# Kernel optimization log

Hardware: AMD Instinct MI355X
Metric: run time of the kernel (lower is better)

Reference implementation:

```python
import jax, jax.numpy as jnp
import numpy as np

NEG = -1e9  # large negative instead of -inf for numerical safety; masked rows are zeroed afterwards
LN_EPS = 1e-5


def layer_norm(x, g, b):
    mu = jnp.mean(x, axis=-1, keepdims=True)
    var = jnp.mean(jnp.square(x - mu), axis=-1, keepdims=True)
    return (x - mu) * jax.lax.rsqrt(var + LN_EPS) * g + b


def causal_conv1d(x_bct, w_oik):
    # x: [B, C, T], w: [O, I, K]; left-pad by K-1 (causal ConvNorm)
    k = w_oik.shape[-1]
    return jax.lax.conv_general_dilated(
        x_bct, w_oik, window_strides=(1,), padding=[(k - 1, 0)],
        dimension_numbers=('NCH', 'OIH', 'NCH'))


def setup_inputs() -> dict:
    key = jax.random.key(0)
    ks = jax.random.split(key, 8)
    B, T, D, H, F, K = 2, 2048, 1024, 16, 4096, 3
    MAXLEN = 4096
    x = jax.random.normal(ks[0], (B, T, D), dtype=jnp.float32)
    lengths = jnp.array([2048, 1536])
    x_mask = jnp.arange(T)[None, :] >= lengths[:, None]  # True = padded
    std = 0.02
    pos_table = jax.random.normal(ks[1], (MAXLEN, D), dtype=jnp.float32) * std
    w_qkv = jax.random.normal(ks[2], (3 * D, D), dtype=jnp.float32) * std
    w_o = jax.random.normal(ks[3], (D, D), dtype=jnp.float32) * std
    conv1_w = jax.random.normal(ks[4], (F, D, K), dtype=jnp.float32) * std
    conv2_w = jax.random.normal(ks[5], (D, F, K), dtype=jnp.float32) * std
    return {
        'x': x, 'x_mask': x_mask, 'pos_table': pos_table,
        'w_qkv': w_qkv, 'w_o': w_o,
        'ln1_g': jnp.ones((D,)), 'ln1_b': jnp.zeros((D,)),
        'ln2_g': jnp.ones((D,)), 'ln2_b': jnp.zeros((D,)),
        'conv1_w': conv1_w, 'conv2_w': conv2_w,
    }


def reference(x, x_mask, pos_table, w_qkv, w_o, ln1_g, ln1_b, ln2_g, ln2_b, conv1_w, conv2_w):
    B, T, D = x.shape
    H = 16
    dh = D // H
    scale = dh ** -0.5

    # ---- self-attention block (pre-norm) ----
    q_in = layer_norm(x, ln1_g, ln1_b)
    q_in = q_in + pos_table[:T][None]  # learnable positional embeddings
    qkv = jnp.einsum('btd,ed->bte', q_in, w_qkv).reshape(B, T, 3, H, dh)
    q, k, v = qkv[:, :, 0], qkv[:, :, 1], qkv[:, :, 2]
    scores = jnp.einsum('bthd,bshd->bhts', q, k) * scale  # [B,H,T,T]
    pad_mask = x_mask[:, None, :, None]                    # mask padded query rows
    causal = jnp.tril(jnp.ones((T, T), dtype=bool))[None, None]
    scores = jnp.where(pad_mask | ~causal, NEG, scores)
    prob = jax.nn.softmax(scores, axis=-1)
    prob = jnp.where(pad_mask, 0.0, prob)
    y = jnp.einsum('bhts,bshd->bthd', prob, v).reshape(B, T, D)
    y = jnp.einsum('btd,ed->bte', y, w_o)
    x = x + y  # dropout p=0

    # ---- positionwise causal conv FFN (pre-norm) ----
    h = layer_norm(x, ln2_g, ln2_b)
    h = jnp.transpose(h, (0, 2, 1))           # [B, D, T]
    h = causal_conv1d(h, conv1_w)             # [B, F, T]
    h = jax.nn.gelu(h, approximate=True)
    h = causal_conv1d(h, conv2_w)             # [B, D, T]
    h = jnp.transpose(h, (0, 2, 1))
    x = x + h
    return x
```

## Files before the change

kernel.cpp:

```cpp
#include <hip/hip_runtime.h>
#include <stdint.h>
#include <math.h>

#define T_SEQ 2048
#define D_MODEL 1024
#define NHEAD 16
#define DH 64
#define F_FF 4096
#define TP (T_SEQ + 2)

typedef unsigned short u16;
typedef float f32x4 __attribute__((ext_vector_type(4)));
typedef __bf16 bf16x8 __attribute__((ext_vector_type(8)));

__device__ __forceinline__ u16 f2bf(float f){
  unsigned u = __float_as_uint(f);
  u = u + 0x7fffu + ((u >> 16) & 1u);
  return (u16)(u >> 16);
}
__device__ __forceinline__ float b2f(u16 h){ return __uint_as_float(((unsigned)h) << 16); }

__device__ __forceinline__ float gelu_f(float x){
  const float c = 0.7978845608028654f;
  float u = c * (x + 0.044715f * x * x * x);
  float e = __expf(-2.0f * u);
  return x * __builtin_amdgcn_rcpf(1.0f + e);
}

#define AS1 __attribute__((address_space(1)))
#define AS3 __attribute__((address_space(3)))
__device__ __forceinline__ void async_cp16(void* lds, const void* g){
  __builtin_amdgcn_global_load_lds((AS1 void*)(void*)g, (AS3 void*)lds, 16, 0, 0);
}

__device__ __forceinline__ float fload(const void* p, size_t i, unsigned isbf){
  return isbf ? b2f(((const u16*)p)[i]) : ((const float*)p)[i];
}

__global__ void detect_dtype(const u16* __restrict__ x, unsigned* __restrict__ flags){
  unsigned e = ((unsigned)x[threadIdx.x] >> 7) & 0xFF;
  bool good = (e == 0 || (e >= 90 && e <= 150));
  unsigned long long b = __ballot(good);
  if (threadIdx.x == 0) flags[0] = (b == ~0ULL) ? 1u : 0u;
}

__global__ __launch_bounds__(256) void canon_mask(const unsigned char* __restrict__ raw,
                                                  unsigned char* __restrict__ canon){
  int i = blockIdx.x * 256 + threadIdx.x;
  if (i >= 2 * T_SEQ) return;
  unsigned char v;
  if (raw[3584]) {
    v = raw[i] != 0;
  } else if (raw[7168]) {
    v = ((const u16*)raw)[i] != 0;
  } else if (raw[14336]) {
    v = ((const int*)raw)[i] != 0;
  } else {
    v = ((const long long*)raw)[i] != 0;
  }
  canon[i] = v;
}

__global__ __launch_bounds__(256)
void cast_any2bf(const void* __restrict__ in, u16* __restrict__ out, int n,
                 const unsigned* __restrict__ flags){
  int i = (blockIdx.x * 256 + threadIdx.x) * 4;
  if (i >= n) return;
  if (flags[0]){
    *(ushort4*)(out + i) = *(const ushort4*)((const u16*)in + i);
  } else {
    float4 v = *(const float4*)((const float*)in + i);
    ushort4 o = { f2bf(v.x), f2bf(v.y), f2bf(v.z), f2bf(v.w) };
    *(ushort4*)(out + i) = o;
  }
}

__global__ __launch_bounds__(256)
void cast_out(const float* __restrict__ in, const float* __restrict__ res,
              void* __restrict__ out, int n, const unsigned* __restrict__ flags){
  int i = (blockIdx.x * 256 + threadIdx.x) * 4;
  if (i >= n) return;
  float4 v = *(const float4*)(in + i);
  float4 r = *(const float4*)(res + i);
  v.x += r.x; v.y += r.y; v.z += r.z; v.w += r.w;
  if (flags[0]){
    ushort4 o = { f2bf(v.x), f2bf(v.y), f2bf(v.z), f2bf(v.w) };
    *(ushort4*)((u16*)out + i) = o;
  } else {
    *(float4*)((float*)out + i) = v;
  }
}

template<int INX1>
__global__ __launch_bounds__(256)
void ln_kernel(const void* __restrict__ inv, const void* __restrict__ g,
               const void* __restrict__ be, const void* __restrict__ pos,
               u16* __restrict__ out, int addpos, int padout,
               const unsigned* __restrict__ flags)
{
  const unsigned isbf = flags[0];
  const int r = blockIdx.x;
  const int bb = r >> 11, tt = r & (T_SEQ - 1);
  const size_t ib = (size_t)r * D_MODEL + threadIdx.x * 4;
  float v0, v1, v2, v3;
  if (INX1){
    float4 v = *(const float4*)((const float*)inv + ib);
    v0 = v.x; v1 = v.y; v2 = v.z; v3 = v.w;
  } else if (isbf){
    ushort4 u = *(const ushort4*)((const u16*)inv + ib);
    v0 = b2f(u.x); v1 = b2f(u.y); v2 = b2f(u.z); v3 = b2f(u.w);
  } else {
    float4 v = *(const float4*)((const float*)inv + ib);
    v0 = v.x; v1 = v.y; v2 = v.z; v3 = v.w;
  }
  float s  = v0 + v1 + v2 + v3;
  float s2 = v0*v0 + v1*v1 + v2*v2 + v3*v3;
  #pragma unroll
  for (int o = 1; o < 64; o <<= 1){ s += __shfl_xor(s, o); s2 += __shfl_xor(s2, o); }
  __shared__ float w1[4], w2[4];
  int w = threadIdx.x >> 6;
  if ((threadIdx.x & 63) == 0){ w1[w] = s; w2[w] = s2; }
  __syncthreads();
  float S  = w1[0] + w1[1] + w1[2] + w1[3];
  float S2 = w2[0] + w2[1] + w2[2] + w2[3];
  float mu  = S * (1.f / 1024.f);
  float var = S2 * (1.f / 1024.f) - mu * mu;
  float rs  = rsqrtf(var + 1e-5f);
  int d0 = threadIdx.x * 4;
  float o0 = (v0 - mu) * rs * fload(g, d0 + 0, isbf) + fload(be, d0 + 0, isbf);
  float o1 = (v1 - mu) * rs * fload(g, d0 + 1, isbf) + fload(be, d0 + 1, isbf);
  float o2 = (v2 - mu) * rs * fload(g, d0 + 2, isbf) + fload(be, d0 + 2, isbf);
  float o3 = (v3 - mu) * rs * fload(g, d0 + 3, isbf) + fload(be, d0 + 3, isbf);
  if (addpos){
    size_t pb = (size_t)tt * D_MODEL + d0;
    o0 += fload(pos, pb + 0, isbf);
    o1 += fload(pos, pb + 1, isbf);
    o2 += fload(pos, pb + 2, isbf);
    o3 += fload(pos, pb + 3, isbf);
  }
  size_t orow = padout ? ((size_t)bb * TP + tt + 2) * (size_t)D_MODEL
                       : (size_t)r * D_MODEL;
  ushort4 ov = { f2bf(o0), f2bf(o1), f2bf(o2), f2bf(o3) };
  *(ushort4*)(out + orow + d0) = ov;
}

__global__ __launch_bounds__(256)
void conv_w_split(const void* __restrict__ in, u16* __restrict__ out, int lg2C,
                  const unsigned* __restrict__ flags){
  int i = blockIdx.x * 256 + threadIdx.x;
  if (i >= 4096 * 1024) return;
  const unsigned isbf = flags[0];
  const int C = 1 << lg2C;
  int c = i & (C - 1);
  size_t sb = (size_t)i * 3;
  size_t ob = (size_t)(i >> lg2C) * 3 * C + c;
  out[ob]         = f2bf(fload(in, sb + 0, isbf));
  out[ob + C]     = f2bf(fload(in, sb + 1, isbf));
  out[ob + 2 * C] = f2bf(fload(in, sb + 2, isbf));
}

__global__ __launch_bounds__(256)
void zero_pads(u16* __restrict__ h2pad, u16* __restrict__ g1pad){
  int tid = blockIdx.x * 256 + threadIdx.x;
  if (tid < 2 * 2 * D_MODEL){
    int b = tid >> 11; int off = tid & (2 * D_MODEL - 1);
    h2pad[(size_t)b * TP * D_MODEL + off] = 0;
  }
  if (tid < 2 * 2 * F_FF){
    int b = tid >> 13; int off = tid & (2 * F_FF - 1);
    g1pad[(size_t)b * TP * F_FF + off] = 0;
  }
}

__device__ __forceinline__ int swz(int tid){
  return (tid & 3) ^ ((tid >> 2) & 3) ^ ((tid >> 4) & 3);
}

template<int MODE>
__global__ __launch_bounds__(256)
void gemm_bt(const u16* __restrict__ A, const u16* __restrict__ B,
             const void* __restrict__ res, void* __restrict__ outp,
             int N, int Kin, int lg2Kin, int nseg, long Abstride,
             const unsigned* __restrict__ flags)
{
  __shared__ u16 smA[128 * 32];
  __shared__ u16 smB[128 * 32];
  const int tid = threadIdx.x;
  const int m0 = blockIdx.y * 128;
  const int n0 = blockIdx.x * 128;
  const int Ktot = Kin * nseg;

  const int ch = swz(tid);
  long abase[2]; const u16* bbase[2];
  #pragma unroll
  for (int i = 0; i < 2; ++i){
    int r = m0 + i * 64 + (tid >> 2);
    int bb = r >> 11, tt = r & (T_SEQ - 1);
    abase[i] = (long)bb * Abstride + (long)tt * Kin + ch * 8;
    bbase[i] = B + (long)(n0 + i * 64 + (tid >> 2)) * Ktot + ch * 8;
  }

  f32x4 acc[4][4];
  #pragma unroll
  for (int i = 0; i < 4; ++i)
    #pragma unroll
    for (int j = 0; j < 4; ++j){ f32x4 z = {0.f,0.f,0.f,0.f}; acc[i][j] = z; }

  const int wm = (tid >> 6) & 1, wn = (tid >> 7) & 1;
  const int lane = tid & 63, lq = lane >> 4, lr = lane & 15;
  const int xq = lq ^ (lr & 3) ^ (lr >> 2);
  const int aoff = (wm * 64 + lr) * 32 + xq * 8;
  const int boff = (wn * 64 + lr) * 32 + xq * 8;

  for (int k0 = 0; k0 < Ktot; k0 += 32){
    int seg = k0 >> lg2Kin;
    int j0  = k0 & (Kin - 1);
    long aso = (long)seg * Kin + j0;
    long bso = k0;
    #pragma unroll
    for (int i = 0; i < 2; ++i){
      async_cp16(&smA[i * 2048 + tid * 8], A + abase[i] + aso);
      async_cp16(&smB[i * 2048 + tid * 8], bbase[i] + bso);
    }
    __syncthreads();
    bf16x8 af[4], bfv[4];
    #pragma unroll
    for (int mi = 0; mi < 4; ++mi) af[mi]  = *(const bf16x8*)&smA[aoff + mi * 512];
    #pragma unroll
    for (int ni = 0; ni < 4; ++ni) bfv[ni] = *(const bf16x8*)&smB[boff + ni * 512];
    #pragma unroll
    for (int mi = 0; mi < 4; ++mi)
      #pragma unroll
      for (int ni = 0; ni < 4; ++ni)
        acc[mi][ni] = __builtin_amdgcn_mfma_f32_16x16x32_bf16(af[mi], bfv[ni], acc[mi][ni], 0, 0, 0);
    __syncthreads();
  }

  const unsigned isbf = (MODE == 1 || MODE == 3) ? flags[0] : 0;
  #pragma unroll
  for (int mi = 0; mi < 4; ++mi){
    #pragma unroll
    for (int ni = 0; ni < 4; ++ni){
      int row0 = m0 + wm * 64 + mi * 16 + lq * 4;
      int col  = n0 + wn * 64 + ni * 16 + lr;
      if (MODE == 0){
        ushort4 pv = { f2bf(acc[mi][ni][0]), f2bf(acc[mi][ni][1]),
                       f2bf(acc[mi][ni][2]), f2bf(acc[mi][ni][3]) };
        if (col < 2 * D_MODEL){
          #pragma unroll
          for (int rr = 0; rr < 4; ++rr)
            ((u16*)outp)[(size_t)(row0 + rr) * N + col] = ((const u16*)&pv)[rr];
        } else {
          int hh = (col - 2 * D_MODEL) >> 6, dd = (col - 2 * D_MODEL) & 63;
          int bb = row0 >> 11, tt = row0 & (T_SEQ - 1);
          *(ushort4*)((u16*)const_cast<void*>(res) +
                      ((size_t)(bb * NHEAD + hh) * 64 + dd) * T_SEQ + tt) = pv;
        }
      } else {
        #pragma unroll
        for (int rr = 0; rr < 4; ++rr){
          int row = row0 + rr;
          float v = acc[mi][ni][rr];
          size_t idx = (size_t)row * N + col;
          if (MODE == 1){
            ((float*)outp)[idx] = v + fload(res, idx, isbf);
          } else if (MODE == 3){
            float ov = v + ((const float*)res)[idx];
            if (isbf) ((u16*)outp)[idx] = f2bf(ov);
            else      ((float*)outp)[idx] = ov;
          }
        }
      }
    }
  }
}

__device__ __forceinline__ void ktile8(
    f32x4 (&acc)[8][4], u16 (*L)[16384], int buf, int abase, int bbase,
    const u16* __restrict__ A, const long (&asrc)[2], const u16* const (&bsrc)[2],
    const int (&adst)[2], const int (&bdst)[2], int kt, bool stage_ok)
{
  const u16* Lp = L[buf];
  u16* Ld = L[(kt + 3) & 3];
  bf16x8 bfr[4], a0[4], a1[4];
  #pragma unroll
  for (int nf = 0; nf < 4; ++nf) bfr[nf] = *(const bf16x8*)&Lp[bbase + nf * 512];
  #pragma unroll
  for (int j = 0; j < 4; ++j) a0[j] = *(const bf16x8*)&Lp[abase + j * 512];
  if (stage_ok){
    #pragma unroll
    for (int s = 0; s < 2; ++s)
      async_cp16(&Ld[adst[s]], A + asrc[s] + (long)(kt + 3) * 32);
  }
  #pragma unroll
  for (int j = 0; j < 4; ++j) a1[j] = *(const bf16x8*)&Lp[abase + (4 + j) * 512];
  if (stage_ok){
    #pragma unroll
    for (int s = 0; s < 2; ++s)
      async_cp16(&Ld[bdst[s]], bsrc[s] + (long)(kt + 3) * 32);
  }
  __builtin_amdgcn_s_setprio(1);
  #pragma unroll
  for (int j = 0; j < 4; ++j)
    #pragma unroll
    for (int nf = 0; nf < 4; ++nf)
      acc[j][nf] = __builtin_amdgcn_mfma_f32_16x16x32_bf16(a0[j], bfr[nf], acc[j][nf], 0, 0, 0);
  #pragma unroll
  for (int j = 0; j < 4; ++j)
    #pragma unroll
    for (int nf = 0; nf < 4; ++nf)
      acc[4 + j][nf] = __builtin_amdgcn_mfma_f32_16x16x32_bf16(a1[j], bfr[nf], acc[4 + j][nf], 0, 0, 0);
  __builtin_amdgcn_s_setprio(0);
}

template<int MODE>
__global__ __launch_bounds__(512, 2)
void gemm8(const u16* __restrict__ A, const u16* __restrict__ Bm,
           void* __restrict__ outp, int N, int Kin, int Ktot, int nkt, long Abstride)
{
  __shared__ u16 L[4][16384];
  const int tid = threadIdx.x;

  const int bid = blockIdx.x;
  const int xcd = bid & 7, idx = bid >> 3;
  int bx, by, kz;
  if (MODE == 2){ bx = 2 * xcd + (idx & 1); by = idx >> 1; kz = 0; }
  else          { kz = xcd >> 1; bx = idx & 3; by = ((xcd & 1) << 3) + (idx >> 2); }
  const int m0 = by * 256, n0 = bx * 256;
  const int kt0 = kz * nkt;
  const int ktEnd = kt0 + nkt;

  const int rl = tid >> 2;
  const int ch = swz(tid);
  long asrc[2]; const u16* bsrc[2]; int adst[2], bdst[2];
  #pragma unroll
  for (int s = 0; s < 2; ++s){
    int r = m0 + s * 128 + rl;
    int bb = r >> 11, tt = r & (T_SEQ - 1);
    asrc[s] = (long)bb * Abstride + (long)tt * Kin + ch * 8;
    bsrc[s] = Bm + (long)(n0 + s * 128 + rl) * Ktot + ch * 8;
    adst[s] = (s * 512 + tid) * 8;
    bdst[s] = 8192 + adst[s];
  }

  const int w = tid >> 6, lane = tid & 63;
  const int wm = w >> 2, wn = w & 3;
  const int quad = lane >> 4, lr = lane & 15;
  const int xq = quad ^ (lr & 3) ^ (lr >> 2);
  const int abase = ((wm * 128 + lr) * 4 + xq) * 8;
  const int bbase = 8192 + ((wn * 64 + lr) * 4 + xq) * 8;

  f32x4 acc[8][4];
  #pragma unroll
  for (int i = 0; i < 8; ++i)
    #pragma unroll
    for (int j = 0; j < 4; ++j){ f32x4 z = {0.f,0.f,0.f,0.f}; acc[i][j] = z; }

  #pragma unroll
  for (int j = 0; j < 3; ++j){
    #pragma unroll
    for (int s = 0; s < 2; ++s) async_cp16(&L[(kt0 + j) & 3][adst[s]], A + asrc[s] + (long)(kt0 + j) * 32);
    #pragma unroll
    for (int s = 0; s < 2; ++s) async_cp16(&L[(kt0 + j) & 3][bdst[s]], bsrc[s] + (long)(kt0 + j) * 32);
  }

  int kt = kt0;
  for (; kt < ktEnd - 2; ++kt){
    asm volatile("s_waitcnt vmcnt(8)" ::: "memory");
    __builtin_amdgcn_s_barrier();
    __builtin_amdgcn_sched_barrier(0);
    ktile8(acc, L, kt & 3, abase, bbase, A, asrc, bsrc, adst, bdst, kt, kt + 3 < ktEnd);
  }
  asm volatile("s_waitcnt vmcnt(4)" ::: "memory");
  __builtin_amdgcn_s_barrier();
  __builtin_amdgcn_sched_barrier(0);
  ktile8(acc, L, (ktEnd - 2) & 3, abase, bbase, A, asrc, bsrc, adst, bdst, ktEnd - 2, false);
  asm volatile("s_waitcnt vmcnt(0)" ::: "memory");
  __builtin_amdgcn_s_barrier();
  __builtin_amdgcn_sched_barrier(0);
  ktile8(acc, L, (ktEnd - 1) & 3, abase, bbase, A, asrc, bsrc, adst, bdst, ktEnd - 1, false);

  #pragma unroll
  for (int mf = 0; mf < 8; ++mf){
    #pragma unroll
    for (int nf = 0; nf < 4; ++nf){
      int col = n0 + wn * 64 + nf * 16 + lr;
      #pragma unroll
      for (int rr = 0; rr < 4; ++rr){
        int row = m0 + wm * 128 + mf * 16 + quad * 4 + rr;
        if (MODE == 2){
          int bb = row >> 11, tt = row & (T_SEQ - 1);
          ((u16*)outp)[((size_t)(bb * TP + tt + 2)) * N + col] = f2bf(gelu_f(acc[mf][nf][rr]));
        } else {
          atomicAdd((float*)outp + (size_t)row * N + col, acc[mf][nf][rr]);
        }
      }
    }
  }
}

__global__ __launch_bounds__(256)
void attn_mfma(const u16* __restrict__ qkv, const u16* __restrict__ vT,
               const unsigned char* __restrict__ mask, u16* __restrict__ y)
{
  const int qb = blockIdx.x, h = blockIdx.y, b = blockIdx.z;
  const int q0 = qb * 64;
  const int tid = threadIdx.x;

  if (mask[b * T_SEQ + q0]){
    int r = tid >> 2, c4 = (tid & 3) * 16;
    u16* yp = y + (size_t)(b * T_SEQ + q0 + r) * D_MODEL + h * DH + c4;
    ushort4 z = {0, 0, 0, 0};
    #pragma unroll
    for (int c = 0; c < 4; ++c) *(ushort4*)(yp + c * 4) = z;
    return;
  }

  const int w = tid >> 6, lane = tid & 63;
  const int quad = lane >> 4, lr = lane & 15;

  __shared__ u16 Ks[64 * 72];
  __shared__ u16 Vs[64 * 72];
  __shared__ u16 Ps[64 * 72];

  bf16x8 aq0, aq1;
  {
    const u16* qp = qkv + (size_t)(b * T_SEQ + q0 + w * 16 + lr) * 3072 + h * DH + quad * 8;
    aq0 = *(const bf16x8*)qp;
    aq1 = *(const bf16x8*)(qp + 32);
  }

  f32x4 acc_o[4];
  #pragma unroll
  for (int i = 0; i < 4; ++i){ f32x4 z = {0.f,0.f,0.f,0.f}; acc_o[i] = z; }
  float mrow[4] = {-1e30f, -1e30f, -1e30f, -1e30f};
  float lrow[4] = {0.f, 0.f, 0.f, 0.f};

  const int sr = tid >> 3, sg = tid & 7;

  for (int it = 0; it <= qb; ++it){
    const int s0 = it * 64;
    #pragma unroll
    for (int rr = 0; rr < 64; rr += 32){
      int row = sr + rr;
      *(uint4*)&Ks[row * 72 + sg * 8] =
        *(const uint4*)(qkv + (size_t)(b * T_SEQ + s0 + row) * 3072 + D_MODEL + h * DH + sg * 8);
      *(uint4*)&Vs[row * 72 + sg * 8] =
        *(const uint4*)(vT + ((size_t)(b * NHEAD + h) * 64 + row) * T_SEQ + s0 + sg * 8);
    }
    __syncthreads();

    f32x4 accs[4];
    #pragma unroll
    for (int nt = 0; nt < 4; ++nt){
      f32x4 z = {0.f, 0.f, 0.f, 0.f};
      bf16x8 bk0 = *(const bf16x8*)&Ks[(nt * 16 + lr) * 72 + quad * 8];
      bf16x8 bk1 = *(const bf16x8*)&Ks[(nt * 16 + lr) * 72 + quad * 8 + 32];
      z = __builtin_amdgcn_mfma_f32_16x16x32_bf16(aq0, bk0, z, 0, 0, 0);
      z = __builtin_amdgcn_mfma_f32_16x16x32_bf16(aq1, bk1, z, 0, 0, 0);
      accs[nt] = z;
    }

    const bool diag = (it == qb);
    float sv[4][4], mx[4];
    #pragma unroll
    for (int rr = 0; rr < 4; ++rr) mx[rr] = -1e30f;
    #pragma unroll
    for (int nt = 0; nt < 4; ++nt){
      #pragma unroll
      for (int rr = 0; rr < 4; ++rr){
        float s = accs[nt][rr] * 0.125f;
        if (diag && (nt * 16 + lr) > (w * 16 + quad * 4 + rr)) s = -1e30f;
        sv[nt][rr] = s;
        mx[rr] = fmaxf(mx[rr], s);
      }
    }
    #pragma unroll
    for (int o = 1; o < 16; o <<= 1){
      #pragma unroll
      for (int rr = 0; rr < 4; ++rr) mx[rr] = fmaxf(mx[rr], __shfl_xor(mx[rr], o));
    }
    float alpha[4], psum[4];
    #pragma unroll
    for (int rr = 0; rr < 4; ++rr){
      float mnew = fmaxf(mrow[rr], mx[rr]);
      alpha[rr] = __expf(mrow[rr] - mnew);
      mrow[rr] = mnew;
      psum[rr] = 0.f;
    }
    #pragma unroll
    for (int nt = 0; nt < 4; ++nt){
      #pragma unroll
      for (int rr = 0; rr < 4; ++rr){
        float p = __expf(sv[nt][rr] - mrow[rr]);
        psum[rr] += p;
        Ps[(w * 16 + quad * 4 + rr) * 72 + nt * 16 + lr] = f2bf(p);
      }
    }
    #pragma unroll
    for (int o = 1; o < 16; o <<= 1){
      #pragma unroll
      for (int rr = 0; rr < 4; ++rr) psum[rr] += __shfl_xor(psum[rr], o);
    }
    #pragma unroll
    for (int rr = 0; rr < 4; ++rr) lrow[rr] = lrow[rr] * alpha[rr] + psum[rr];
    #pragma unroll
    for (int nt = 0; nt < 4; ++nt)
      #pragma unroll
      for (int rr = 0; rr < 4; ++rr) acc_o[nt][rr] *= alpha[rr];

    bf16x8 ap0 = *(const bf16x8*)&Ps[(w * 16 + lr) * 72 + quad * 8];
    bf16x8 ap1 = *(const bf16x8*)&Ps[(w * 16 + lr) * 72 + quad * 8 + 32];
    #pragma unroll
    for (int nt = 0; nt < 4; ++nt){
      bf16x8 bv0 = *(const bf16x8*)&Vs[(nt * 16 + lr) * 72 + quad * 8];
      bf16x8 bv1 = *(const bf16x8*)&Vs[(nt * 16 + lr) * 72 + quad * 8 + 32];
      acc_o[nt] = __builtin_amdgcn_mfma_f32_16x16x32_bf16(ap0, bv0, acc_o[nt], 0, 0, 0);
      acc_o[nt] = __builtin_amdgcn_mfma_f32_16x16x32_bf16(ap1, bv1, acc_o[nt], 0, 0, 0);
    }
    __syncthreads();
  }

  #pragma unroll
  for (int rr = 0; rr < 4; ++rr){
    int qg = q0 + w * 16 + quad * 4 + rr;
    float inv = 1.0f / lrow[rr];
    bool rm = mask[b * T_SEQ + qg] != 0;
    #pragma unroll
    for (int nt = 0; nt < 4; ++nt){
      float v = rm ? 0.f : acc_o[nt][rr] * inv;
      y[(size_t)(b * T_SEQ + qg) * D_MODEL + h * DH + nt * 16 + lr] = f2bf(v);
    }
  }
}

extern "C" void kernel_launch(void* const* d_in, const int* in_sizes, int n_in,
                              void* d_out, int out_size, void* d_ws, size_t ws_size,
                              hipStream_t stream)
{
  const void* x       = d_in[0];
  const unsigned char* xmask_raw = (const unsigned char*)d_in[1];
  const void* pos     = d_in[2];
  const void* w_qkv   = d_in[3];
  const void* w_o     = d_in[4];
  const void* ln1_g   = d_in[5];
  const void* ln1_b   = d_in[6];
  const void* ln2_g   = d_in[7];
  const void* ln2_b   = d_in[8];
  const void* conv1_w = d_in[9];
  const void* conv2_w = d_in[10];

  char* ws = (char*)d_ws;
  size_t o = 0;
  auto alloc = [&](size_t bytes){ size_t cur = o; o += (bytes + 255) & ~(size_t)255; return cur; };
  unsigned* flags = (unsigned*)(ws + alloc(256));
  unsigned char* maskc = (unsigned char*)(ws + alloc(2 * T_SEQ));
  float* x1   = (float*)(ws + alloc((size_t)2 * T_SEQ * D_MODEL * 4));
  char* h2slab = ws + alloc((size_t)2 * TP * D_MODEL * 2);
  u16* g1pad  = (u16*)(ws + alloc((size_t)2 * TP * F_FF * 2));
  u16* slabA  = (u16*)(ws + alloc((size_t)4096 * 3072 * 2));
  u16* qy     = (u16*)(ws + alloc((size_t)4096 * 1024 * 2));
  char* vslab = ws + alloc((size_t)4096 * 1024 * 4);
  u16* vt     = (u16*)vslab;
  float* xc   = (float*)vslab;

  u16* wqkv_c = (u16*)h2slab;
  u16* wo_c   = (u16*)h2slab + (size_t)3072 * 1024;
  u16* h2pad  = (u16*)h2slab;
  u16* qin    = qy;
  u16* qkvb   = slabA;
  u16* yb     = qy;
  u16* W1cat  = slabA;
  u16* W2cat  = slabA;

  detect_dtype<<<1, 64, 0, stream>>>((const u16*)x, flags);
  canon_mask<<<16, 256, 0, stream>>>(xmask_raw, maskc);
  cast_any2bf<<<3072 * 1024 / 4 / 256, 256, 0, stream>>>(w_qkv, wqkv_c, 3072 * 1024, flags);
  cast_any2bf<<<1024 * 1024 / 4 / 256, 256, 0, stream>>>(w_o, wo_c, 1024 * 1024, flags);
  ln_kernel<0><<<4096, 256, 0, stream>>>(x, ln1_g, ln1_b, pos, qin, 1, 0, flags);
  gemm_bt<0><<<dim3(24, 32), 256, 0, stream>>>(qin, wqkv_c, vt, qkvb,
                                               3072, 1024, 10, 1, (long)T_SEQ * 1024, flags);
  attn_mfma<<<dim3(32, 16, 2), 256, 0, stream>>>(qkvb, vt, maskc, yb);
  gemm_bt<1><<<dim3(8, 32), 256, 0, stream>>>(yb, wo_c, x, x1,
                                              1024, 1024, 10, 1, (long)T_SEQ * 1024, flags);
  hipMemsetAsync(xc, 0, (size_t)4096 * 1024 * 4, stream);
  conv_w_split<<<4096 * 1024 / 256, 256, 0, stream>>>(conv1_w, W1cat, 10, flags);
  zero_pads<<<64, 256, 0, stream>>>(h2pad, g1pad);
  ln_kernel<1><<<4096, 256, 0, stream>>>(x1, ln2_g, ln2_b, nullptr, h2pad, 0, 1, flags);
  gemm8<2><<<dim3(256, 1, 1), 512, 0, stream>>>(h2pad, W1cat, g1pad,
                                                4096, 1024, 3072, 96, (long)TP * 1024);
  conv_w_split<<<4096 * 1024 / 256, 256, 0, stream>>>(conv2_w, W2cat, 12, flags);
  gemm8<4><<<dim3(256, 1, 1), 512, 0, stream>>>(g1pad, W2cat, xc,
                                                1024, 4096, 12288, 96, (long)TP * 4096);
  cast_out<<<4096 * 1024 / 4 / 256, 256, 0, stream>>>(xc, x1, d_out, 4096 * 1024, flags);
}
```

Measured before the change: 657.6 us.

## Replace 256x256 quad-buffered conv GEMM with 128x128 double-buffered tiles

Swaps the 512-thread, 256x256-tile GEMM with a 4-stage async LDS pipeline for a 256-thread, 128x128-tile kernel using two LDS buffers and a full vmcnt(0) wait each k-step. The grid grows from 256 to 1024 blocks and launch bounds allow four blocks per CU. The aim is more occupancy and better CU load balance. In exchange each tile reuses less data, global traffic rises, and the shallower pipeline exposes more load latency. The split-K with atomics and the fused GELU epilogue are kept.

```diff
diff --git a/kernel.cpp b/kernel.cpp
--- a/kernel.cpp
+++ b/kernel.cpp
@@ -275,124 +275,93 @@
   }
 }
 
-__device__ __forceinline__ void ktile8(
-    f32x4 (&acc)[8][4], u16 (*L)[16384], int buf, int abase, int bbase,
-    const u16* __restrict__ A, const long (&asrc)[2], const u16* const (&bsrc)[2],
-    const int (&adst)[2], const int (&bdst)[2], int kt, bool stage_ok)
-{
-  const u16* Lp = L[buf];
-  u16* Ld = L[(kt + 3) & 3];
-  bf16x8 bfr[4], a0[4], a1[4];
-  #pragma unroll
-  for (int nf = 0; nf < 4; ++nf) bfr[nf] = *(const bf16x8*)&Lp[bbase + nf * 512];
-  #pragma unroll
-  for (int j = 0; j < 4; ++j) a0[j] = *(const bf16x8*)&Lp[abase + j * 512];
-  if (stage_ok){
-    #pragma unroll
-    for (int s = 0; s < 2; ++s)
-      async_cp16(&Ld[adst[s]], A + asrc[s] + (long)(kt + 3) * 32);
-  }
-  #pragma unroll
-  for (int j = 0; j < 4; ++j) a1[j] = *(const bf16x8*)&Lp[abase + (4 + j) * 512];
-  if (stage_ok){
-    #pragma unroll
-    for (int s = 0; s < 2; ++s)
-      async_cp16(&Ld[bdst[s]], bsrc[s] + (long)(kt + 3) * 32);
-  }
-  __builtin_amdgcn_s_setprio(1);
-  #pragma unroll
-  for (int j = 0; j < 4; ++j)
-    #pragma unroll
-    for (int nf = 0; nf < 4; ++nf)
-      acc[j][nf] = __builtin_amdgcn_mfma_f32_16x16x32_bf16(a0[j], bfr[nf], acc[j][nf], 0, 0, 0);
-  #pragma unroll
-  for (int j = 0; j < 4; ++j)
-    #pragma unroll
-    for (int nf = 0; nf < 4; ++nf)
-      acc[4 + j][nf] = __builtin_amdgcn_mfma_f32_16x16x32_bf16(a1[j], bfr[nf], acc[4 + j][nf], 0, 0, 0);
-  __builtin_amdgcn_s_setprio(0);
-}
-
 template<int MODE>
-__global__ __launch_bounds__(512, 2)
-void gemm8(const u16* __restrict__ A, const u16* __restrict__ Bm,
+__global__ __launch_bounds__(256, 4)
+void gemm4(const u16* __restrict__ A, const u16* __restrict__ Bm,
            void* __restrict__ outp, int N, int Kin, int Ktot, int nkt, long Abstride)
 {
-  __shared__ u16 L[4][16384];
+  __shared__ u16 L[2][8192];
   const int tid = threadIdx.x;
 
   const int bid = blockIdx.x;
   const int xcd = bid & 7, idx = bid >> 3;
   int bx, by, kz;
-  if (MODE == 2){ bx = 2 * xcd + (idx & 1); by = idx >> 1; kz = 0; }
-  else          { kz = xcd >> 1; bx = idx & 3; by = ((xcd & 1) << 3) + (idx >> 2); }
-  const int m0 = by * 256, n0 = bx * 256;
+  if (MODE == 2){ bx = xcd * 4 + (idx & 3); by = idx >> 2; kz = 0; }
+  else          { kz = xcd >> 1; bx = idx & 7; by = ((xcd & 1) << 4) + (idx >> 3); }
+  const int m0 = by * 128, n0 = bx * 128;
   const int kt0 = kz * nkt;
   const int ktEnd = kt0 + nkt;
 
-  const int rl = tid >> 2;
   const int ch = swz(tid);
-  long asrc[2]; const u16* bsrc[2]; int adst[2], bdst[2];
-  #pragma unroll
-  for (int s = 0; s < 2; ++s){
-    int r = m0 + s * 128 + rl;
+  int asrc[2]; const u16* bsrc[2];
+  #pragma unroll
+  for (int i = 0; i < 2; ++i){
+    int r = m0 + i * 64 + (tid >> 2);
     int bb = r >> 11, tt = r & (T_SEQ - 1);
-    asrc[s] = (long)bb * Abstride + (long)tt * Kin + ch * 8;
-    bsrc[s] = Bm + (long)(n0 + s * 128 + rl) * Ktot + ch * 8;
-    adst[s] = (s * 512 + tid) * 8;
-    bdst[s] = 8192 + adst[s];
+    asrc[i] = bb * (int)Abstride + tt * Kin + ch * 8;
+    bsrc[i] = Bm + (long)(n0 + i * 64 + (tid >> 2)) * Ktot + ch * 8;
   }
 
   const int w = tid >> 6, lane = tid & 63;
-  const int wm = w >> 2, wn = w & 3;
+  const int wm = w >> 1, wn = w & 1;
   const int quad = lane >> 4, lr = lane & 15;
   const int xq = quad ^ (lr & 3) ^ (lr >> 2);
-  const int abase = ((wm * 128 + lr) * 4 + xq) * 8;
-  const int bbase = 8192 + ((wn * 64 + lr) * 4 + xq) * 8;
-
-  f32x4 acc[8][4];
-  #pragma unroll
-  for (int i = 0; i < 8; ++i)
+  const int aoff = (wm * 64 + lr) * 32 + xq * 8;
+  const int boff = 4096 + (wn * 64 + lr) * 32 + xq * 8;
+
+  f32x4 acc[4][4];
+  #pragma unroll
+  for (int i = 0; i < 4; ++i)
     #pragma unroll
     for (int j = 0; j < 4; ++j){ f32x4 z = {0.f,0.f,0.f,0.f}; acc[i][j] = z; }
 
   #pragma unroll
-  for (int j = 0; j < 3; ++j){
-    #pragma unroll
-    for (int s = 0; s < 2; ++s) async_cp16(&L[(kt0 + j) & 3][adst[s]], A + asrc[s] + (long)(kt0 + j) * 32);
-    #pragma unroll
-    for (int s = 0; s < 2; ++s) async_cp16(&L[(kt0 + j) & 3][bdst[s]], bsrc[s] + (long)(kt0 + j) * 32);
-  }
-
-  int kt = kt0;
-  for (; kt < ktEnd - 2; ++kt){
-    asm volatile("s_waitcnt vmcnt(8)" ::: "memory");
+  for (int i = 0; i < 2; ++i){
+    async_cp16(&L[0][i * 2048 + tid * 8], A + asrc[i] + (long)kt0 * 32);
+    async_cp16(&L[0][4096 + i * 2048 + tid * 8], bsrc[i] + (long)kt0 * 32);
+  }
+
+  for (int kt = kt0; kt < ktEnd; ++kt){
+    const int b = (kt - kt0) & 1;
+    asm volatile("s_waitcnt vmcnt(0)" ::: "memory");
     __builtin_amdgcn_s_barrier();
     __builtin_amdgcn_sched_barrier(0);
-    ktile8(acc, L, kt & 3, abase, bbase, A, asrc, bsrc, adst, bdst, kt, kt + 3 < ktEnd);
-  }
-  asm volatile("s_waitcnt vmcnt(4)" ::: "memory");
-  __builtin_amdgcn_s_barrier();
-  __builtin_amdgcn_sched_barrier(0);
-  ktile8(acc, L, (ktEnd - 2) & 3, abase, bbase, A, asrc, bsrc, adst, bdst, ktEnd - 2, false);
-  asm volatile("s_waitcnt vmcnt(0)" ::: "memory");
-  __builtin_amdgcn_s_barrier();
-  __builtin_amdgcn_sched_barrier(0);
-  ktile8(acc, L, (ktEnd - 1) & 3, abase, bbase, A, asrc, bsrc, adst, bdst, ktEnd - 1, false);
-
-  #pragma unroll
-  for (int mf = 0; mf < 8; ++mf){
-    #pragma unroll
-    for (int nf = 0; nf < 4; ++nf){
-      int col = n0 + wn * 64 + nf * 16 + lr;
+    const u16* Lp = L[b];
+    bf16x8 af[4], bfv[4];
+    #pragma unroll
+    for (int mi = 0; mi < 4; ++mi) af[mi]  = *(const bf16x8*)&Lp[aoff + mi * 512];
+    #pragma unroll
+    for (int ni = 0; ni < 4; ++ni) bfv[ni] = *(const bf16x8*)&Lp[boff + ni * 512];
+    if (kt + 1 < ktEnd){
+      u16* Ld = L[b ^ 1];
+      #pragma unroll
+      for (int i = 0; i < 2; ++i){
+        async_cp16(&Ld[i * 2048 + tid * 8], A + asrc[i] + (long)(kt + 1) * 32);
+        async_cp16(&Ld[4096 + i * 2048 + tid * 8], bsrc[i] + (long)(kt + 1) * 32);
+      }
+    }
+    __builtin_amdgcn_s_setprio(1);
+    #pragma unroll
+    for (int mi = 0; mi < 4; ++mi)
+      #pragma unroll
+      for (int ni = 0; ni < 4; ++ni)
+        acc[mi][ni] = __builtin_amdgcn_mfma_f32_16x16x32_bf16(af[mi], bfv[ni], acc[mi][ni], 0, 0, 0);
+    __builtin_amdgcn_s_setprio(0);
+  }
+
+  #pragma unroll
+  for (int mi = 0; mi < 4; ++mi){
+    #pragma unroll
+    for (int ni = 0; ni < 4; ++ni){
+      int col = n0 + wn * 64 + ni * 16 + lr;
       #pragma unroll
       for (int rr = 0; rr < 4; ++rr){
-        int row = m0 + wm * 128 + mf * 16 + quad * 4 + rr;
+        int row = m0 + wm * 64 + mi * 16 + quad * 4 + rr;
         if (MODE == 2){
           int bb = row >> 11, tt = row & (T_SEQ - 1);
-          ((u16*)outp)[((size_t)(bb * TP + tt + 2)) * N + col] = f2bf(gelu_f(acc[mf][nf][rr]));
+          ((u16*)outp)[((size_t)(bb * TP + tt + 2)) * N + col] = f2bf(gelu_f(acc[mi][ni][rr]));
         } else {
-          atomicAdd((float*)outp + (size_t)row * N + col, acc[mf][nf][rr]);
+          atomicAdd((float*)outp + (size_t)row * N + col, acc[mi][ni][rr]);
         }
       }
     }
@@ -587,10 +556,10 @@
   conv_w_split<<<4096 * 1024 / 256, 256, 0, stream>>>(conv1_w, W1cat, 10, flags);
   zero_pads<<<64, 256, 0, stream>>>(h2pad, g1pad);
   ln_kernel<1><<<4096, 256, 0, stream>>>(x1, ln2_g, ln2_b, nullptr, h2pad, 0, 1, flags);
-  gemm8<2><<<dim3(256, 1, 1), 512, 0, stream>>>(h2pad, W1cat, g1pad,
-                                                4096, 1024, 3072, 96, (long)TP * 1024);
+  gemm4<2><<<dim3(1024, 1, 1), 256, 0, stream>>>(h2pad, W1cat, g1pad,
+                                                 4096, 1024, 3072, 96, (long)TP * 1024);
   conv_w_split<<<4096 * 1024 / 256, 256, 0, stream>>>(conv2_w, W2cat, 12, flags);
-  gemm8<4><<<dim3(256, 1, 1), 512, 0, stream>>>(g1pad, W2cat, xc,
-                                                1024, 4096, 12288, 96, (long)TP * 4096);
+  gemm4<4><<<dim3(1024, 1, 1), 256, 0, stream>>>(g1pad, W2cat, xc,
+                                                 1024, 4096, 12288, 96, (long)TP * 4096);
   cast_out<<<4096 * 1024 / 4 / 256, 256, 0, stream>>>(xc, x1, d_out, 4096 * 1024, flags);
 }
```

New measurement: 695.6 us. 1.06x slower.
